# Performance work log

Measured on AMD Instinct MI355X. Metric: run time of the kernel, lower is better.

Reference implementation:

```python
import jax, jax.numpy as jnp
import numpy as np

NL, D, DI, N, R, K = 32, 256, 512, 16, 16, 4   # layers, d_model, d_inner, d_state, dt_rank, d_conv
V, FF, BATCH, L = 4096, 1024, 32, 256


def _mamba_layer(x, p):
    # x: (B, L, D). One pre-norm Mamba block with residual: x + mamba(LN(x)).
    ln_w, ln_b, in_w, cw, cb, xp_w, dtw, dtb, A_log, Dskip, out_w = p
    mu = x.mean(-1, keepdims=True)
    var = ((x - mu) ** 2).mean(-1, keepdims=True)
    h = (x - mu) / jnp.sqrt(var + 1e-5) * ln_w + ln_b
    xz = jnp.einsum('bld,ed->ble', h, in_w)            # (B, L, 2*DI)
    xm, z = jnp.split(xz, 2, axis=-1)
    seq = xm.shape[1]
    # causal depthwise conv1d, kernel K, then SiLU
    xpad = jnp.pad(xm, ((0, 0), (K - 1, 0), (0, 0)))
    xc = sum(xpad[:, k:k + seq] * cw[:, k] for k in range(K)) + cb
    xc = jax.nn.silu(xc)
    dbc = jnp.einsum('ble,fe->blf', xc, xp_w)          # (B, L, R+2N)
    dt, Bm, Cm = jnp.split(dbc, [R, R + N], axis=-1)
    dt = jax.nn.softplus(jnp.einsum('blr,er->ble', dt, dtw) + dtb)  # (B, L, DI)
    A = -jnp.exp(A_log)                                # (DI, N)

    def step(hs, inp):
        dt_t, B_t, C_t, x_t = inp                      # (B,DI),(B,N),(B,N),(B,DI)
        dA = jnp.exp(dt_t[..., None] * A)              # (B, DI, N)
        hs = hs * dA + (dt_t * x_t)[..., None] * B_t[:, None, :]
        return hs, jnp.einsum('ben,bn->be', hs, C_t)

    h0 = jnp.zeros((xc.shape[0], DI, N), xc.dtype)
    _, ys = jax.lax.scan(step, h0, (dt.swapaxes(0, 1), Bm.swapaxes(0, 1), Cm.swapaxes(0, 1), xc.swapaxes(0, 1)))
    y = ys.swapaxes(0, 1) + xc * Dskip
    y = y * jax.nn.silu(z)
    return x + jnp.einsum('ble,de->bld', y, out_w)


def _stack_forward(x, params):
    return jax.lax.scan(lambda c, p: (jax.checkpoint(_mamba_layer)(c, p), None), x, params)[0]


def setup_inputs() -> dict:
    key = jax.random.key(0)
    ks = jax.random.split(key, 12)
    rn = lambda k, shape, s=0.02: jax.random.normal(k, shape, jnp.float32) * s
    return {
        'token_ids': jax.random.randint(ks[0], (BATCH, L), 0, V),
        'emb': rn(ks[1], (V, D)),
        'ln_w': jnp.ones((NL, D)), 'ln_b': jnp.zeros((NL, D)),
        'in_proj_w': rn(ks[2], (NL, 2 * DI, D)),
        'conv_w': rn(ks[3], (NL, DI, K), 0.1), 'conv_b': jnp.zeros((NL, DI)),
        'x_proj_w': rn(ks[4], (NL, R + 2 * N, DI)),
        'dt_w': rn(ks[5], (NL, DI, R), 0.1),
        'dt_b': jnp.full((NL, DI), float(np.log(np.expm1(0.01))), jnp.float32),
        'A_log': jnp.broadcast_to(jnp.log(jnp.arange(1, N + 1, dtype=jnp.float32)), (NL, DI, N)) + 0.0,
        'Dskip': jnp.ones((NL, DI)),
        'out_proj_w': rn(ks[6], (NL, D, DI)),
        'W1': rn(ks[7], (FF, D)), 'b1': jnp.zeros((FF,)),
        'W2': rn(ks[8], (V, FF)), 'b2': jnp.zeros((V,)),
    }


def reference(token_ids, emb, ln_w, ln_b, in_proj_w, conv_w, conv_b, x_proj_w, dt_w, dt_b, A_log, Dskip, out_proj_w, W1, b1, W2, b2):
    x = emb[token_ids]                                  # (B, L, D)
    params = (ln_w, ln_b, in_proj_w, conv_w, conv_b, x_proj_w, dt_w, dt_b, A_log, Dskip, out_proj_w)
    x = _stack_forward(x, params)                       # 32 stacked Mamba blocks
    h = jax.nn.relu(x @ W1.T + b1)
    return h @ W2.T + b2                                # (B, L, V) logits
```

## Files before the change

kernel.cpp:

```cpp
#include <hip/hip_runtime.h>
#include <hip/hip_bf16.h>
#include <cstdint>
#include <cstddef>


typedef __bf16 v8bf __attribute__((ext_vector_type(8)));
typedef float  v4f  __attribute__((ext_vector_type(4)));

__device__ __forceinline__ void async_copy16(const void* g, void* l) {
  __builtin_amdgcn_global_load_lds((const __attribute__((address_space(1))) void*)g,
                                   (__attribute__((address_space(3))) void*)l, 16, 0, 0);
}

__device__ __forceinline__ float bf(__bf16 v) { return (float)v; }

constexpr size_t OFF_WIN  = 0;
constexpr size_t OFF_WXP  = 16777216;
constexpr size_t OFF_WOUT = 18350080;
constexpr size_t OFF_WW1  = 26738688;
constexpr size_t OFF_WW2  = 27262976;
constexpr size_t OFF_X    = 35651584;
constexpr size_t OFF_H    = 44040192;
constexpr size_t OFF_XZ   = 48234496;
constexpr size_t OFF_DBC  = 65011712;
constexpr size_t OFF_PART = 66584576;
constexpr size_t OFF_SS   = 82313216;
constexpr size_t OFF_A2   = 83296256;

__global__ __launch_bounds__(256)
void f2b_multi(const float* __restrict__ s0, const float* __restrict__ s1,
               const float* __restrict__ s2, const float* __restrict__ s3,
               const float* __restrict__ s4, const float* __restrict__ s5,
               char* __restrict__ ws) {
  size_t i = (size_t)blockIdx.x * 256 + threadIdx.x;
  if (i < 8388608) { ((__bf16*)(ws + OFF_WIN))[i] = (__bf16)s0[i]; return; }
  i -= 8388608;
  if (i < 786432)  { ((__bf16*)(ws + OFF_WXP))[i] = (__bf16)s1[i]; return; }
  i -= 786432;
  if (i < 4194304) { ((__bf16*)(ws + OFF_WOUT))[i] = (__bf16)s2[i]; return; }
  i -= 4194304;
  if (i < 262144)  { ((__bf16*)(ws + OFF_WW1))[i] = (__bf16)s3[i]; return; }
  i -= 262144;
  if (i < 4194304) { ((__bf16*)(ws + OFF_WW2))[i] = (__bf16)s4[i]; return; }
  i -= 4194304;
  ((float*)(ws + OFF_A2))[i] = -1.4426950408889634f * __expf(s5[i]);
}

__global__ __launch_bounds__(256) void f2b_k(const float* __restrict__ X,
                                             __bf16* __restrict__ O) {
  size_t i = (size_t)blockIdx.x * 256 + threadIdx.x;
  O[i] = (__bf16)X[i];
}

__global__ __launch_bounds__(256)
void embed_ln_k(const int* __restrict__ tok, const float* __restrict__ emb,
                const float* __restrict__ w, const float* __restrict__ b,
                float* __restrict__ X, __bf16* __restrict__ H) {
  int row = blockIdx.x;
  int t   = threadIdx.x;
  float v = emb[(size_t)tok[row] * 256 + t];
  X[(size_t)row * 256 + t] = v;
  float s = v, q = v * v;
  #pragma unroll
  for (int o = 32; o > 0; o >>= 1) { s += __shfl_xor(s, o); q += __shfl_xor(q, o); }
  __shared__ float ss[4], qq[4];
  int wv = t >> 6;
  if ((t & 63) == 0) { ss[wv] = s; qq[wv] = q; }
  __syncthreads();
  s = ss[0] + ss[1] + ss[2] + ss[3];
  q = qq[0] + qq[1] + qq[2] + qq[3];
  float mu  = s * (1.f / 256.f);
  float var = q * (1.f / 256.f) - mu * mu;
  float r   = rsqrtf(var + 1e-5f);
  H[(size_t)row * 256 + t] = (__bf16)((v - mu) * r * w[t] + b[t]);
}

template <int EPI>
__global__ __launch_bounds__(256, 2)
void gemm_bt(const __bf16* __restrict__ A, const __bf16* __restrict__ W,
             void* outp, const float* __restrict__ bias, int M, int N, int K) {
  __shared__ __align__(16) __bf16 sA[128 * 32];
  __shared__ __align__(16) __bf16 sB[128 * 32];
  const int tid  = threadIdx.x;
  const int bm0  = blockIdx.y << 7;
  const int bn0  = blockIdx.x << 7;
  const int lane = tid & 63;
  const int wv   = tid >> 6;
  const int wm   = (wv >> 1) << 6;
  const int wn   = (wv & 1) << 6;
  const int lr   = lane & 15;
  const int lk   = lane >> 4;

  v4f acc[4][4] = {};

  const int r0 = tid >> 2;
  const int c0 = (tid & 3) << 3;
  const int wbase = (tid & ~63) << 3;

  const __bf16* gA0 = A + (size_t)(bm0 + r0) * K + c0;
  const __bf16* gA1 = A + (size_t)(bm0 + 64 + r0) * K + c0;
  const __bf16* gB0 = W + (size_t)(bn0 + r0) * K + c0;
  const __bf16* gB1 = W + (size_t)(bn0 + 64 + r0) * K + c0;

  for (int kk = 0; kk < K; kk += 32) {
    async_copy16(gA0 + kk, sA + wbase);
    async_copy16(gA1 + kk, sA + 2048 + wbase);
    async_copy16(gB0 + kk, sB + wbase);
    async_copy16(gB1 + kk, sB + 2048 + wbase);
    __syncthreads();
    v8bf af[4], bfr[4];
    #pragma unroll
    for (int i = 0; i < 4; ++i)
      af[i] = *(const v8bf*)(sA + ((wm + i * 16 + lr) << 5) + (lk << 3));
    #pragma unroll
    for (int j = 0; j < 4; ++j)
      bfr[j] = *(const v8bf*)(sB + ((wn + j * 16 + lr) << 5) + (lk << 3));
    #pragma unroll
    for (int i = 0; i < 4; ++i)
      #pragma unroll
      for (int j = 0; j < 4; ++j)
        acc[i][j] = __builtin_amdgcn_mfma_f32_16x16x32_bf16(af[i], bfr[j], acc[i][j], 0, 0, 0);
    __syncthreads();
  }

  #pragma unroll
  for (int i = 0; i < 4; ++i) {
    #pragma unroll
    for (int j = 0; j < 4; ++j) {
      int gc = bn0 + wn + j * 16 + lr;
      #pragma unroll
      for (int v = 0; v < 4; ++v) {
        int gr = bm0 + wm + i * 16 + (lk << 2) + v;
        float val = acc[i][j][v];
        size_t idx = (size_t)gr * N + gc;
        if (EPI == 0) {
          ((__bf16*)outp)[idx] = (__bf16)val;
        } else if (EPI == 1) {
          val += bias[gc]; val = fmaxf(val, 0.f);
          ((__bf16*)outp)[idx] = (__bf16)val;
        } else {
          ((float*)outp)[idx] = val + bias[gc];
        }
      }
    }
  }
}

__global__ __launch_bounds__(512, 4)
void convscan1_k(const __bf16* __restrict__ XZ,
                 const float* __restrict__ cw, const float* __restrict__ cb,
                 const __bf16* __restrict__ Wxp,
                 const float* __restrict__ dtw, const float* __restrict__ dtb,
                 const float* __restrict__ A2,
                 float* __restrict__ DBC,
                 float* __restrict__ PART, float* __restrict__ SS) {
  __shared__ __align__(16) __bf16 sXC[16 * 512];
  __shared__ __align__(16) float  sDBC[16 * 48];
  const int tid = threadIdx.x;
  const int c   = blockIdx.x >> 5;
  const int b   = blockIdx.x & 31;
  const int bl0 = b * 256 + c * 16;

  {
    const int r  = tid >> 5;
    const int ec = tid & 31;
    #pragma unroll
    for (int j = 0; j < 2; ++j) {
      const int e = (ec << 3) + (j << 8);
      v4f cw4[8];
      #pragma unroll
      for (int jj = 0; jj < 8; ++jj) cw4[jj] = *(const v4f*)(cw + (size_t)(e + jj) * 4);
      float a[8];
      #pragma unroll
      for (int jj = 0; jj < 8; ++jj) a[jj] = cb[e + jj];
      #pragma unroll
      for (int k = 0; k < 4; ++k) {
        if (c > 0 || r + k >= 3) {
          const v8bf xv = *(const v8bf*)(XZ + (size_t)(bl0 + r + k - 3) * 1024 + e);
          #pragma unroll
          for (int jj = 0; jj < 8; ++jj) a[jj] += bf(xv[jj]) * cw4[jj][k];
        }
      }
      v8bf outv;
      #pragma unroll
      for (int jj = 0; jj < 8; ++jj) {
        float s = a[jj] / (1.f + __expf(-a[jj]));
        outv[jj] = (__bf16)s;
      }
      const int cbk = (e >> 3) ^ (r & 7);
      *(v8bf*)(sXC + r * 512 + (cbk << 3)) = outv;
    }
  }
  __syncthreads();

  if (tid < 192) {
    const int w = tid >> 6, lane = tid & 63, lr = lane & 15, lk = lane >> 4;
    v4f acc = {};
    for (int kk = 0; kk < 512; kk += 32) {
      const v8bf bfr = *(const v8bf*)(Wxp + (size_t)(w * 16 + lr) * 512 + kk + (lk << 3));
      const int cbk = (((kk >> 3) + lk) ^ (lr & 7));
      const v8bf af = *(const v8bf*)(sXC + lr * 512 + (cbk << 3));
      acc = __builtin_amdgcn_mfma_f32_16x16x32_bf16(af, bfr, acc, 0, 0, 0);
    }
    const int gc = w * 16 + lr;
    #pragma unroll
    for (int v = 0; v < 4; ++v)
      sDBC[((lk << 2) + v) * 48 + gc] = acc[v];
  }
  __syncthreads();

  if (tid < 192)
    *(v4f*)(DBC + (size_t)bl0 * 48 + tid * 4) = *(const v4f*)(sDBC + tid * 4);

  if (c < 15) {
    const int e = tid;
    v4f a2[4], wd[4];
    #pragma unroll
    for (int q = 0; q < 4; ++q) {
      a2[q] = *(const v4f*)(A2  + (size_t)e * 16 + q * 4);
      wd[q] = *(const v4f*)(dtw + (size_t)e * 16 + q * 4);
    }
    const float bias = dtb[e];
    float part[16];
    #pragma unroll
    for (int n = 0; n < 16; ++n) part[n] = 0.f;
    float S = 0.f;
    for (int tt = 0; tt < 16; ++tt) {
      const v4f* dp = (const v4f*)(sDBC + tt * 48);
      float dtv = bias;
      {
        const v4f d0 = dp[0], d1 = dp[1], d2 = dp[2], d3 = dp[3];
        #pragma unroll
        for (int r = 0; r < 4; ++r)
          dtv += d0[r] * wd[0][r] + d1[r] * wd[1][r] + d2[r] * wd[2][r] + d3[r] * wd[3][r];
      }
      dtv = (dtv > 20.f) ? dtv : log1pf(__expf(dtv));
      const float x = bf(sXC[tt * 512 + (((e >> 3) ^ (tt & 7)) << 3) + (e & 7)]);
      const float dtx = dtv * x;
      S += dtv;
      {
        const v4f bv0 = dp[4], bv1 = dp[5], bv2 = dp[6], bv3 = dp[7];
        #pragma unroll
        for (int v = 0; v < 4; ++v) {
          part[v]      = part[v]      * exp2f(dtv * a2[0][v]) + dtx * bv0[v];
          part[4 + v]  = part[4 + v]  * exp2f(dtv * a2[1][v]) + dtx * bv1[v];
          part[8 + v]  = part[8 + v]  * exp2f(dtv * a2[2][v]) + dtx * bv2[v];
          part[12 + v] = part[12 + v] * exp2f(dtv * a2[3][v]) + dtx * bv3[v];
        }
      }
    }
    const size_t o = (((size_t)c * 32 + b) * 512 + e) * 16;
    #pragma unroll
    for (int rq = 0; rq < 4; ++rq) {
      v4f p;
      #pragma unroll
      for (int v = 0; v < 4; ++v) p[v] = part[rq * 4 + v];
      *(v4f*)(PART + o + rq * 4) = p;
    }
    SS[((size_t)c * 32 + b) * 512 + e] = S;
  }
}

__global__ __launch_bounds__(512, 4)
void scan2out_k(const __bf16* __restrict__ XZ,
                const float* __restrict__ cw, const float* __restrict__ cb,
                const float* __restrict__ DBC,
                const float* __restrict__ dtw, const float* __restrict__ dtb,
                const float* __restrict__ A2, const float* __restrict__ Dskip,
                const float* __restrict__ PART, const float* __restrict__ SS,
                const __bf16* __restrict__ Wout,
                const float* __restrict__ lnw, const float* __restrict__ lnb,
                float* __restrict__ X, __bf16* __restrict__ H) {
  __shared__ __align__(16) __bf16 sY[16 * 520];
  __shared__ __align__(16) __bf16 sB[256 * 32];
  __shared__ float sSum[8][16], sSq[8][16];
  const int tid = threadIdx.x;
  const int c   = blockIdx.x >> 5;
  const int b   = blockIdx.x & 31;
  const int bl0 = b * 256 + c * 16;
  const int e   = tid;

  v4f a2[4], wd[4];
  #pragma unroll
  for (int q = 0; q < 4; ++q) {
    a2[q] = *(const v4f*)(A2  + (size_t)e * 16 + q * 4);
    wd[q] = *(const v4f*)(dtw + (size_t)e * 16 + q * 4);
  }
  const float bias = dtb[e];
  const float Dsk  = Dskip[e];
  const v4f   cwv  = *(const v4f*)(cw + (size_t)e * 4);
  const float cbe  = cb[e];

  float h[16];
  #pragma unroll
  for (int n = 0; n < 16; ++n) h[n] = 0.f;
  for (int cc = 0; cc < c; ++cc) {
    const float S  = SS[((size_t)cc * 32 + b) * 512 + e];
    const size_t o = (((size_t)cc * 32 + b) * 512 + e) * 16;
    #pragma unroll
    for (int rq = 0; rq < 4; ++rq) {
      const v4f p = *(const v4f*)(PART + o + rq * 4);
      #pragma unroll
      for (int v = 0; v < 4; ++v)
        h[rq * 4 + v] = h[rq * 4 + v] * exp2f(a2[rq][v] * S) + p[v];
    }
  }

  float w0 = 0.f, w1 = 0.f, w2 = 0.f;
  if (c > 0) {
    w0 = bf(XZ[(size_t)(bl0 - 3) * 1024 + e]);
    w1 = bf(XZ[(size_t)(bl0 - 2) * 1024 + e]);
    w2 = bf(XZ[(size_t)(bl0 - 1) * 1024 + e]);
  }

  for (int tt = 0; tt < 16; ++tt) {
    const float xt = bf(XZ[(size_t)(bl0 + tt) * 1024 + e]);
    float a = cbe + w0 * cwv[0] + w1 * cwv[1] + w2 * cwv[2] + xt * cwv[3];
    const float x = a / (1.f + __expf(-a));
    w0 = w1; w1 = w2; w2 = xt;
    const v4f* dp = (const v4f*)(DBC + (size_t)(bl0 + tt) * 48);
    float dtv = bias;
    {
      const v4f d0 = dp[0], d1 = dp[1], d2 = dp[2], d3 = dp[3];
      #pragma unroll
      for (int r = 0; r < 4; ++r)
        dtv += d0[r] * wd[0][r] + d1[r] * wd[1][r] + d2[r] * wd[2][r] + d3[r] * wd[3][r];
    }
    dtv = (dtv > 20.f) ? dtv : log1pf(__expf(dtv));
    const float dtx = dtv * x;
    float y = 0.f;
    {
      const v4f bv0 = dp[4], bv1 = dp[5], bv2 = dp[6], bv3 = dp[7];
      const v4f cv0 = dp[8], cv1 = dp[9], cv2 = dp[10], cv3 = dp[11];
      #pragma unroll
      for (int v = 0; v < 4; ++v) {
        h[v]      = h[v]      * exp2f(dtv * a2[0][v]) + dtx * bv0[v];  y += h[v]      * cv0[v];
        h[4 + v]  = h[4 + v]  * exp2f(dtv * a2[1][v]) + dtx * bv1[v];  y += h[4 + v]  * cv1[v];
        h[8 + v]  = h[8 + v]  * exp2f(dtv * a2[2][v]) + dtx * bv2[v];  y += h[8 + v]  * cv2[v];
        h[12 + v] = h[12 + v] * exp2f(dtv * a2[3][v]) + dtx * bv3[v];  y += h[12 + v] * cv3[v];
      }
    }
    const float z  = bf(XZ[(size_t)(bl0 + tt) * 1024 + 512 + e]);
    const float sg = z / (1.f + __expf(-z));
    sY[tt * 520 + e] = (__bf16)((y + x * Dsk) * sg);
  }
  __syncthreads();

  const int w = tid >> 6, lane = tid & 63, lr = lane & 15, lk = lane >> 4;
  const int wn = w << 5;
  v4f acc[2] = {};
  for (int kk = 0; kk < 512; kk += 32) {
    async_copy16(Wout + (size_t)(tid >> 2) * 512 + ((tid & 3) << 3) + kk,
                 sB + ((tid & ~63) << 3));
    async_copy16(Wout + (size_t)(128 + (tid >> 2)) * 512 + ((tid & 3) << 3) + kk,
                 sB + 4096 + ((tid & ~63) << 3));
    __syncthreads();
    const v8bf af = *(const v8bf*)(sY + lr * 520 + kk + (lk << 3));
    #pragma unroll
    for (int j = 0; j < 2; ++j) {
      const v8bf bfr = *(const v8bf*)(sB + ((wn + j * 16 + lr) << 5) + (lk << 3));
      acc[j] = __builtin_amdgcn_mfma_f32_16x16x32_bf16(af, bfr, acc[j], 0, 0, 0);
    }
    __syncthreads();
  }

  float s2[4], q2[4];
  #pragma unroll
  for (int v = 0; v < 4; ++v) {
    const int gr = bl0 + (lk << 2) + v;
    float s = 0.f, q = 0.f;
    #pragma unroll
    for (int j = 0; j < 2; ++j) {
      const int gc = wn + j * 16 + lr;
      float val = X[(size_t)gr * 256 + gc] + acc[j][v];
      acc[j][v] = val;
      s += val; q += val * val;
    }
    #pragma unroll
    for (int o = 8; o > 0; o >>= 1) { s += __shfl_xor(s, o); q += __shfl_xor(q, o); }
    s2[v] = s; q2[v] = q;
  }
  if (lr == 0) {
    #pragma unroll
    for (int v = 0; v < 4; ++v) {
      const int row = (lk << 2) + v;
      sSum[w][row] = s2[v];
      sSq[w][row]  = q2[v];
    }
  }
  __syncthreads();
  #pragma unroll
  for (int v = 0; v < 4; ++v) {
    const int row = (lk << 2) + v;
    float S = 0.f, Q = 0.f;
    #pragma unroll
    for (int ww = 0; ww < 8; ++ww) { S += sSum[ww][row]; Q += sSq[ww][row]; }
    const float mu   = S * (1.f / 256.f);
    const float var  = Q * (1.f / 256.f) - mu * mu;
    const float rinv = rsqrtf(var + 1e-5f);
    const int gr = bl0 + row;
    #pragma unroll
    for (int j = 0; j < 2; ++j) {
      const int gc = wn + j * 16 + lr;
      const float val = acc[j][v];
      X[(size_t)gr * 256 + gc] = val;
      H[(size_t)gr * 256 + gc] = (__bf16)((val - mu) * rinv * lnw[gc] + lnb[gc]);
    }
  }
}

extern "C" void kernel_launch(void* const* d_in, const int* in_sizes, int n_in,
                              void* d_out, int out_size, void* d_ws, size_t ws_size,
                              hipStream_t stream) {
  const int*   tok  = (const int*)d_in[0];
  const float* emb  = (const float*)d_in[1];
  const float* lnw  = (const float*)d_in[2];
  const float* lnb  = (const float*)d_in[3];
  const float* inw  = (const float*)d_in[4];
  const float* cw   = (const float*)d_in[5];
  const float* cb   = (const float*)d_in[6];
  const float* xpw  = (const float*)d_in[7];
  const float* dtw  = (const float*)d_in[8];
  const float* dtb  = (const float*)d_in[9];
  const float* alog = (const float*)d_in[10];
  const float* dsk  = (const float*)d_in[11];
  const float* outw = (const float*)d_in[12];
  const float* W1   = (const float*)d_in[13];
  const float* b1   = (const float*)d_in[14];
  const float* W2   = (const float*)d_in[15];
  const float* b2   = (const float*)d_in[16];

  char* ws = (char*)d_ws;
  __bf16* WIN   = (__bf16*)(ws + OFF_WIN);
  __bf16* WXP   = (__bf16*)(ws + OFF_WXP);
  __bf16* WOUT  = (__bf16*)(ws + OFF_WOUT);
  __bf16* WW1   = (__bf16*)(ws + OFF_WW1);
  __bf16* WW2   = (__bf16*)(ws + OFF_WW2);
  float*  X     = (float*)(ws + OFF_X);
  __bf16* H     = (__bf16*)(ws + OFF_H);
  __bf16* XZ    = (__bf16*)(ws + OFF_XZ);
  float*  DBC   = (float*)(ws + OFF_DBC);
  float*  PART  = (float*)(ws + OFF_PART);
  float*  SS    = (float*)(ws + OFF_SS);
  float*  A2    = (float*)(ws + OFF_A2);
  __bf16* XB    = (__bf16*)(ws + OFF_PART);
  __bf16* HH    = (__bf16*)(ws + OFF_PART + 8388608);

  f2b_multi<<<70656, 256, 0, stream>>>(inw, xpw, outw, W1, W2, alog, ws);
  embed_ln_k<<<8192, 256, 0, stream>>>(tok, emb, lnw, lnb, X, H);

  for (int l = 0; l < 32; ++l) {
    const float*  cw_l   = cw   + (size_t)l * 512 * 4;
    const float*  cb_l   = cb   + (size_t)l * 512;
    const __bf16* xpw_l  = WXP  + (size_t)l * 48 * 512;
    const float*  dtw_l  = dtw  + (size_t)l * 512 * 16;
    const float*  dtb_l  = dtb  + (size_t)l * 512;
    const float*  A2_l   = A2   + (size_t)l * 512 * 16;
    const float*  dsk_l  = dsk  + (size_t)l * 512;
    const __bf16* inw_l  = WIN  + (size_t)l * 1024 * 256;
    const __bf16* outw_l = WOUT + (size_t)l * 256 * 512;
    const int lnx = (l + 1 < 32) ? l + 1 : 31;

    gemm_bt<0><<<dim3(8, 64), 256, 0, stream>>>(H, inw_l, XZ, nullptr, 8192, 1024, 256);
    convscan1_k<<<512, 512, 0, stream>>>(XZ, cw_l, cb_l, xpw_l, dtw_l, dtb_l,
                                         A2_l, DBC, PART, SS);
    scan2out_k<<<512, 512, 0, stream>>>(XZ, cw_l, cb_l, DBC, dtw_l, dtb_l,
                                        A2_l, dsk_l, PART, SS, outw_l,
                                        lnw + (size_t)lnx * 256,
                                        lnb + (size_t)lnx * 256, X, H);
  }

  f2b_k<<<8192, 256, 0, stream>>>(X, XB);
  gemm_bt<1><<<dim3(8, 64), 256, 0, stream>>>(XB, WW1, HH, b1, 8192, 1024, 256);
  gemm_bt<2><<<dim3(32, 64), 256, 0, stream>>>(HH, WW2, (float*)d_out, b2, 8192, 4096, 1024);
}
```

Baseline: 4.244 ms.

## Fuse per-layer Mamba kernels into a persistent megakernel with grid barriers

Replaces the 96 per-layer launches (in_proj GEMM, conv+chunk scan, scan+out_proj) with one persistent kernel of 512 blocks that loops over all 32 layers and separates the phases with a hierarchical atomic grid barrier. The conv/xproj results (xc in fp32, dbc) now stay in shared memory between the chunk-scan phase and the final scan phase, so the DBC global buffer and the conv recomputation go away. The cost is that every block must be co-resident for the barrier to work, and the barrier has a timeout escape that could silently break correctness if that fails. The in_proj GEMM now uses 512-thread blocks computing 128x128 tiles, a different tiling from the old GEMM.

```diff
diff --git a/kernel.cpp b/kernel.cpp
--- a/kernel.cpp
+++ b/kernel.cpp
@@ -22,16 +22,22 @@
 constexpr size_t OFF_X    = 35651584;
 constexpr size_t OFF_H    = 44040192;
 constexpr size_t OFF_XZ   = 48234496;
-constexpr size_t OFF_DBC  = 65011712;
 constexpr size_t OFF_PART = 66584576;
 constexpr size_t OFF_SS   = 82313216;
 constexpr size_t OFF_A2   = 83296256;
+constexpr size_t OFF_BAR  = 84344832;
 
 __global__ __launch_bounds__(256)
 void f2b_multi(const float* __restrict__ s0, const float* __restrict__ s1,
                const float* __restrict__ s2, const float* __restrict__ s3,
                const float* __restrict__ s4, const float* __restrict__ s5,
                char* __restrict__ ws) {
+  if (blockIdx.x == 0) {
+    int* bar = (int*)(ws + OFF_BAR);
+    bar[threadIdx.x] = 0;
+    bar[threadIdx.x + 256] = 0;
+    if (threadIdx.x < 32) bar[threadIdx.x + 512] = 0;
+  }
   size_t i = (size_t)blockIdx.x * 256 + threadIdx.x;
   if (i < 8388608) { ((__bf16*)(ws + OFF_WIN))[i] = (__bf16)s0[i]; return; }
   i -= 8388608;
@@ -146,266 +152,328 @@
   }
 }
 
-__global__ __launch_bounds__(512, 4)
-void convscan1_k(const __bf16* __restrict__ XZ,
-                 const float* __restrict__ cw, const float* __restrict__ cb,
-                 const __bf16* __restrict__ Wxp,
-                 const float* __restrict__ dtw, const float* __restrict__ dtb,
-                 const float* __restrict__ A2,
-                 float* __restrict__ DBC,
-                 float* __restrict__ PART, float* __restrict__ SS) {
-  __shared__ __align__(16) __bf16 sXC[16 * 512];
-  __shared__ __align__(16) float  sDBC[16 * 48];
-  const int tid = threadIdx.x;
-  const int c   = blockIdx.x >> 5;
-  const int b   = blockIdx.x & 31;
-  const int bl0 = b * 256 + c * 16;
-
-  {
-    const int r  = tid >> 5;
-    const int ec = tid & 31;
-    #pragma unroll
-    for (int j = 0; j < 2; ++j) {
-      const int e = (ec << 3) + (j << 8);
-      v4f cw4[8];
-      #pragma unroll
-      for (int jj = 0; jj < 8; ++jj) cw4[jj] = *(const v4f*)(cw + (size_t)(e + jj) * 4);
-      float a[8];
-      #pragma unroll
-      for (int jj = 0; jj < 8; ++jj) a[jj] = cb[e + jj];
-      #pragma unroll
-      for (int k = 0; k < 4; ++k) {
-        if (c > 0 || r + k >= 3) {
-          const v8bf xv = *(const v8bf*)(XZ + (size_t)(bl0 + r + k - 3) * 1024 + e);
-          #pragma unroll
-          for (int jj = 0; jj < 8; ++jj) a[jj] += bf(xv[jj]) * cw4[jj][k];
-        }
-      }
-      v8bf outv;
-      #pragma unroll
-      for (int jj = 0; jj < 8; ++jj) {
-        float s = a[jj] / (1.f + __expf(-a[jj]));
-        outv[jj] = (__bf16)s;
-      }
-      const int cbk = (e >> 3) ^ (r & 7);
-      *(v8bf*)(sXC + r * 512 + (cbk << 3)) = outv;
+__device__ __forceinline__ void gbar(int* BAR, int ph) {
+  __syncthreads();
+  if (threadIdx.x == 0) {
+    __threadfence();
+    int* cg   = BAR + ((blockIdx.x >> 4) << 4);
+    int* root = BAR + 512;
+    int* phs  = BAR + 528;
+    bool last = false;
+    int p = __hip_atomic_fetch_add(cg, 1, __ATOMIC_ACQ_REL, __HIP_MEMORY_SCOPE_AGENT);
+    if (p == 15) {
+      int q = __hip_atomic_fetch_add(root, 1, __ATOMIC_ACQ_REL, __HIP_MEMORY_SCOPE_AGENT);
+      last = (q == 31);
     }
+    if (last) {
+      #pragma unroll 1
+      for (int i = 0; i <= 32; ++i)
+        __hip_atomic_store(BAR + i * 16, 0, __ATOMIC_RELAXED, __HIP_MEMORY_SCOPE_AGENT);
+      __hip_atomic_store(phs, ph, __ATOMIC_RELEASE, __HIP_MEMORY_SCOPE_AGENT);
+    } else {
+      long long t0 = clock64();
+      while (__hip_atomic_load(phs, __ATOMIC_ACQUIRE, __HIP_MEMORY_SCOPE_AGENT) < ph) {
+        if (clock64() - t0 > 5000000LL) break;
+      }
+    }
+    __threadfence();
   }
   __syncthreads();
-
-  if (tid < 192) {
-    const int w = tid >> 6, lane = tid & 63, lr = lane & 15, lk = lane >> 4;
-    v4f acc = {};
-    for (int kk = 0; kk < 512; kk += 32) {
-      const v8bf bfr = *(const v8bf*)(Wxp + (size_t)(w * 16 + lr) * 512 + kk + (lk << 3));
-      const int cbk = (((kk >> 3) + lk) ^ (lr & 7));
-      const v8bf af = *(const v8bf*)(sXC + lr * 512 + (cbk << 3));
-      acc = __builtin_amdgcn_mfma_f32_16x16x32_bf16(af, bfr, acc, 0, 0, 0);
+}
+
+struct MegaP {
+  const __bf16 *WIN, *WXP, *WOUT;
+  const float *cw, *cb, *dtw, *dtb, *A2v, *dsk, *lnw, *lnb;
+  float *X; __bf16 *H; __bf16 *XZ; float *PART; float *SS; int *BAR;
+};
+
+__global__ __launch_bounds__(512, 4) void mamba_mega(MegaP P) {
+  __shared__ __align__(16) char sMem[69888];
+  __bf16* const sXC  = (__bf16*)sMem;
+  __bf16* const sY   = (__bf16*)sMem;
+  float*  const sXCf = (float*)(sMem + 16640);
+  float*  const sDBC = (float*)(sMem + 49408);
+  __bf16* const sB3  = (__bf16*)(sMem + 52480);
+  float*  const sSum = (float*)(sMem + 68864);
+  float*  const sSq  = (float*)(sMem + 69376);
+  __bf16* const sA1  = (__bf16*)sMem;
+  __bf16* const sB1  = (__bf16*)(sMem + 8192);
+
+  const int tid = threadIdx.x;
+  const int bid = blockIdx.x;
+  const int c   = bid >> 5, b = bid & 31;
+  const int bl0 = b * 256 + c * 16;
+  const int bm0 = (bid >> 3) << 7;
+  const int bn0 = (bid & 7) << 7;
+  const int lane = tid & 63, wv = tid >> 6;
+  const int lr = lane & 15, lk = lane >> 4;
+  int ph = 0;
+
+  for (int l = 0; l < 32; ++l) {
+    const __bf16* Wi  = P.WIN  + (size_t)l * 262144;
+    const __bf16* Wx  = P.WXP  + (size_t)l * 24576;
+    const __bf16* Wo  = P.WOUT + (size_t)l * 131072;
+    const float* cwL  = P.cw  + (size_t)l * 2048;
+    const float* cbL  = P.cb  + (size_t)l * 512;
+    const float* dtwL = P.dtw + (size_t)l * 8192;
+    const float* dtbL = P.dtb + (size_t)l * 512;
+    const float* A2L  = P.A2v + (size_t)l * 8192;
+    const float* dskL = P.dsk + (size_t)l * 512;
+    const int lnx = (l + 1 < 32) ? l + 1 : 31;
+    const float* lnwL = P.lnw + (size_t)lnx * 256;
+    const float* lnbL = P.lnb + (size_t)lnx * 256;
+
+    {
+      const int wm  = (wv >> 2) << 6;
+      const int wnc = (((wv >> 1) & 1) << 6) + ((wv & 1) << 5);
+      v4f acc[4][2] = {};
+      const int r0 = tid >> 2, c0 = (tid & 3) << 3;
+      const int wbase = (tid & ~63) << 3;
+      const __bf16* gA = P.H + (size_t)(bm0 + r0) * 256 + c0;
+      const __bf16* gB = Wi  + (size_t)(bn0 + r0) * 256 + c0;
+      for (int kk = 0; kk < 256; kk += 32) {
+        async_copy16(gA + kk, sA1 + wbase);
+        async_copy16(gB + kk, sB1 + wbase);
+        __syncthreads();
+        v8bf af[4], bfr[2];
+        #pragma unroll
+        for (int i = 0; i < 4; ++i)
+          af[i] = *(const v8bf*)(sA1 + ((wm + i * 16 + lr) << 5) + (lk << 3));
+        #pragma unroll
+        for (int j = 0; j < 2; ++j)
+          bfr[j] = *(const v8bf*)(sB1 + ((wnc + j * 16 + lr) << 5) + (lk << 3));
+        #pragma unroll
+        for (int i = 0; i < 4; ++i)
+          #pragma unroll
+          for (int j = 0; j < 2; ++j)
+            acc[i][j] = __builtin_amdgcn_mfma_f32_16x16x32_bf16(af[i], bfr[j], acc[i][j], 0, 0, 0);
+        __syncthreads();
+      }
+      #pragma unroll
+      for (int i = 0; i < 4; ++i)
+        #pragma unroll
+        for (int j = 0; j < 2; ++j)
+          #pragma unroll
+          for (int v = 0; v < 4; ++v)
+            P.XZ[(size_t)(bm0 + wm + i * 16 + (lk << 2) + v) * 1024 +
+                 (bn0 + wnc + j * 16 + lr)] = (__bf16)acc[i][j][v];
     }
-    const int gc = w * 16 + lr;
-    #pragma unroll
-    for (int v = 0; v < 4; ++v)
-      sDBC[((lk << 2) + v) * 48 + gc] = acc[v];
-  }
-  __syncthreads();
-
-  if (tid < 192)
-    *(v4f*)(DBC + (size_t)bl0 * 48 + tid * 4) = *(const v4f*)(sDBC + tid * 4);
-
-  if (c < 15) {
-    const int e = tid;
-    v4f a2[4], wd[4];
-    #pragma unroll
-    for (int q = 0; q < 4; ++q) {
-      a2[q] = *(const v4f*)(A2  + (size_t)e * 16 + q * 4);
-      wd[q] = *(const v4f*)(dtw + (size_t)e * 16 + q * 4);
+    gbar(P.BAR, ++ph);
+
+    {
+      const int r = tid >> 5, ec = tid & 31;
+      #pragma unroll
+      for (int j = 0; j < 2; ++j) {
+        const int e = (ec << 3) + (j << 8);
+        v4f cw4[8];
+        #pragma unroll
+        for (int jj = 0; jj < 8; ++jj) cw4[jj] = *(const v4f*)(cwL + (size_t)(e + jj) * 4);
+        float a[8];
+        #pragma unroll
+        for (int jj = 0; jj < 8; ++jj) a[jj] = cbL[e + jj];
+        #pragma unroll
+        for (int k = 0; k < 4; ++k) {
+          if (c > 0 || r + k >= 3) {
+            const v8bf xv = *(const v8bf*)(P.XZ + (size_t)(bl0 + r + k - 3) * 1024 + e);
+            #pragma unroll
+            for (int jj = 0; jj < 8; ++jj) a[jj] += bf(xv[jj]) * cw4[jj][k];
+          }
+        }
+        v8bf outv; v4f f0, f1;
+        #pragma unroll
+        for (int jj = 0; jj < 8; ++jj) {
+          const float s = a[jj] / (1.f + __expf(-a[jj]));
+          outv[jj] = (__bf16)s;
+          if (jj < 4) f0[jj] = s; else f1[jj - 4] = s;
+        }
+        const int cbk = (e >> 3) ^ (r & 7);
+        *(v8bf*)(sXC + r * 512 + (cbk << 3)) = outv;
+        *(v4f*)(sXCf + r * 512 + e)     = f0;
+        *(v4f*)(sXCf + r * 512 + e + 4) = f1;
+      }
+      __syncthreads();
+      if (tid < 192) {
+        const int w = tid >> 6;
+        v4f acc = {};
+        for (int kk = 0; kk < 512; kk += 32) {
+          const v8bf bfr = *(const v8bf*)(Wx + (size_t)(w * 16 + lr) * 512 + kk + (lk << 3));
+          const int cbk = (((kk >> 3) + lk) ^ (lr & 7));
+          const v8bf af = *(const v8bf*)(sXC + lr * 512 + (cbk << 3));
+          acc = __builtin_amdgcn_mfma_f32_16x16x32_bf16(af, bfr, acc, 0, 0, 0);
+        }
+        const int gc = w * 16 + lr;
+        #pragma unroll
+        for (int v = 0; v < 4; ++v)
+          sDBC[((lk << 2) + v) * 48 + gc] = acc[v];
+      }
+      __syncthreads();
+      if (c < 15) {
+        const int e = tid;
+        v4f a2v[4], wd[4];
+        #pragma unroll
+        for (int q = 0; q < 4; ++q) {
+          a2v[q] = *(const v4f*)(A2L  + (size_t)e * 16 + q * 4);
+          wd[q]  = *(const v4f*)(dtwL + (size_t)e * 16 + q * 4);
+        }
+        const float bias = dtbL[e];
+        float part[16];
+        #pragma unroll
+        for (int n = 0; n < 16; ++n) part[n] = 0.f;
+        float S = 0.f;
+        for (int tt = 0; tt < 16; ++tt) {
+          const v4f* dp = (const v4f*)(sDBC + tt * 48);
+          float dtv = bias;
+          {
+            const v4f d0 = dp[0], d1 = dp[1], d2 = dp[2], d3 = dp[3];
+            #pragma unroll
+            for (int r2 = 0; r2 < 4; ++r2)
+              dtv += d0[r2] * wd[0][r2] + d1[r2] * wd[1][r2] + d2[r2] * wd[2][r2] + d3[r2] * wd[3][r2];
+          }
+          dtv = (dtv > 20.f) ? dtv : log1pf(__expf(dtv));
+          const float x = sXCf[tt * 512 + e];
+          const float dtx = dtv * x;
+          S += dtv;
+          {
+            const v4f bv0 = dp[4], bv1 = dp[5], bv2 = dp[6], bv3 = dp[7];
+            #pragma unroll
+            for (int v = 0; v < 4; ++v) {
+              part[v]      = part[v]      * exp2f(dtv * a2v[0][v]) + dtx * bv0[v];
+              part[4 + v]  = part[4 + v]  * exp2f(dtv * a2v[1][v]) + dtx * bv1[v];
+              part[8 + v]  = part[8 + v]  * exp2f(dtv * a2v[2][v]) + dtx * bv2[v];
+              part[12 + v] = part[12 + v] * exp2f(dtv * a2v[3][v]) + dtx * bv3[v];
+            }
+          }
+        }
+        const size_t o = (((size_t)c * 32 + b) * 512 + e) * 16;
+        #pragma unroll
+        for (int rq = 0; rq < 4; ++rq) {
+          v4f p;
+          #pragma unroll
+          for (int v = 0; v < 4; ++v) p[v] = part[rq * 4 + v];
+          *(v4f*)(P.PART + o + rq * 4) = p;
+        }
+        P.SS[((size_t)c * 32 + b) * 512 + e] = S;
+      }
     }
-    const float bias = dtb[e];
-    float part[16];
-    #pragma unroll
-    for (int n = 0; n < 16; ++n) part[n] = 0.f;
-    float S = 0.f;
-    for (int tt = 0; tt < 16; ++tt) {
-      const v4f* dp = (const v4f*)(sDBC + tt * 48);
-      float dtv = bias;
-      {
-        const v4f d0 = dp[0], d1 = dp[1], d2 = dp[2], d3 = dp[3];
-        #pragma unroll
-        for (int r = 0; r < 4; ++r)
-          dtv += d0[r] * wd[0][r] + d1[r] * wd[1][r] + d2[r] * wd[2][r] + d3[r] * wd[3][r];
-      }
-      dtv = (dtv > 20.f) ? dtv : log1pf(__expf(dtv));
-      const float x = bf(sXC[tt * 512 + (((e >> 3) ^ (tt & 7)) << 3) + (e & 7)]);
-      const float dtx = dtv * x;
-      S += dtv;
-      {
-        const v4f bv0 = dp[4], bv1 = dp[5], bv2 = dp[6], bv3 = dp[7];
+    gbar(P.BAR, ++ph);
+
+    {
+      const int e = tid;
+      v4f a2v[4], wd[4];
+      #pragma unroll
+      for (int q = 0; q < 4; ++q) {
+        a2v[q] = *(const v4f*)(A2L  + (size_t)e * 16 + q * 4);
+        wd[q]  = *(const v4f*)(dtwL + (size_t)e * 16 + q * 4);
+      }
+      const float bias = dtbL[e];
+      const float Dsk  = dskL[e];
+      float h[16];
+      #pragma unroll
+      for (int n = 0; n < 16; ++n) h[n] = 0.f;
+      for (int cc = 0; cc < c; ++cc) {
+        const float S  = P.SS[((size_t)cc * 32 + b) * 512 + e];
+        const size_t o = (((size_t)cc * 32 + b) * 512 + e) * 16;
+        #pragma unroll
+        for (int rq = 0; rq < 4; ++rq) {
+          const v4f p = *(const v4f*)(P.PART + o + rq * 4);
+          #pragma unroll
+          for (int v = 0; v < 4; ++v)
+            h[rq * 4 + v] = h[rq * 4 + v] * exp2f(a2v[rq][v] * S) + p[v];
+        }
+      }
+      for (int tt = 0; tt < 16; ++tt) {
+        const float x = sXCf[tt * 512 + e];
+        const v4f* dp = (const v4f*)(sDBC + tt * 48);
+        float dtv = bias;
+        {
+          const v4f d0 = dp[0], d1 = dp[1], d2 = dp[2], d3 = dp[3];
+          #pragma unroll
+          for (int r2 = 0; r2 < 4; ++r2)
+            dtv += d0[r2] * wd[0][r2] + d1[r2] * wd[1][r2] + d2[r2] * wd[2][r2] + d3[r2] * wd[3][r2];
+        }
+        dtv = (dtv > 20.f) ? dtv : log1pf(__expf(dtv));
+        const float dtx = dtv * x;
+        float y = 0.f;
+        {
+          const v4f bv0 = dp[4], bv1 = dp[5], bv2 = dp[6], bv3 = dp[7];
+          const v4f cv0 = dp[8], cv1 = dp[9], cv2 = dp[10], cv3 = dp[11];
+          #pragma unroll
+          for (int v = 0; v < 4; ++v) {
+            h[v]      = h[v]      * exp2f(dtv * a2v[0][v]) + dtx * bv0[v];  y += h[v]      * cv0[v];
+            h[4 + v]  = h[4 + v]  * exp2f(dtv * a2v[1][v]) + dtx * bv1[v];  y += h[4 + v]  * cv1[v];
+            h[8 + v]  = h[8 + v]  * exp2f(dtv * a2v[2][v]) + dtx * bv2[v];  y += h[8 + v]  * cv2[v];
+            h[12 + v] = h[12 + v] * exp2f(dtv * a2v[3][v]) + dtx * bv3[v];  y += h[12 + v] * cv3[v];
+          }
+        }
+        const float z  = bf(P.XZ[(size_t)(bl0 + tt) * 1024 + 512 + e]);
+        const float sg = z / (1.f + __expf(-z));
+        sY[tt * 520 + e] = (__bf16)((y + x * Dsk) * sg);
+      }
+      __syncthreads();
+
+      const int wn = wv << 5;
+      v4f acc[2] = {};
+      for (int kk = 0; kk < 512; kk += 32) {
+        async_copy16(Wo + (size_t)(tid >> 2) * 512 + ((tid & 3) << 3) + kk,
+                     sB3 + ((tid & ~63) << 3));
+        async_copy16(Wo + (size_t)(128 + (tid >> 2)) * 512 + ((tid & 3) << 3) + kk,
+                     sB3 + 4096 + ((tid & ~63) << 3));
+        __syncthreads();
+        const v8bf af = *(const v8bf*)(sY + lr * 520 + kk + (lk << 3));
+        #pragma unroll
+        for (int j = 0; j < 2; ++j) {
+          const v8bf bfr = *(const v8bf*)(sB3 + ((wn + j * 16 + lr) << 5) + (lk << 3));
+          acc[j] = __builtin_amdgcn_mfma_f32_16x16x32_bf16(af, bfr, acc[j], 0, 0, 0);
+        }
+        __syncthreads();
+      }
+
+      float s2[4], q2[4];
+      #pragma unroll
+      for (int v = 0; v < 4; ++v) {
+        const int gr = bl0 + (lk << 2) + v;
+        float s = 0.f, q = 0.f;
+        #pragma unroll
+        for (int j = 0; j < 2; ++j) {
+          const int gc = wn + j * 16 + lr;
+          float val = P.X[(size_t)gr * 256 + gc] + acc[j][v];
+          acc[j][v] = val;
+          s += val; q += val * val;
+        }
+        #pragma unroll
+        for (int o = 8; o > 0; o >>= 1) { s += __shfl_xor(s, o); q += __shfl_xor(q, o); }
+        s2[v] = s; q2[v] = q;
+      }
+      if (lr == 0) {
         #pragma unroll
         for (int v = 0; v < 4; ++v) {
-          part[v]      = part[v]      * exp2f(dtv * a2[0][v]) + dtx * bv0[v];
-          part[4 + v]  = part[4 + v]  * exp2f(dtv * a2[1][v]) + dtx * bv1[v];
-          part[8 + v]  = part[8 + v]  * exp2f(dtv * a2[2][v]) + dtx * bv2[v];
-          part[12 + v] = part[12 + v] * exp2f(dtv * a2[3][v]) + dtx * bv3[v];
-        }
-      }
+          const int row = (lk << 2) + v;
+          sSum[wv * 16 + row] = s2[v];
+          sSq[wv * 16 + row]  = q2[v];
+        }
+      }
+      __syncthreads();
+      #pragma unroll
+      for (int v = 0; v < 4; ++v) {
+        const int row = (lk << 2) + v;
+        float S = 0.f, Q = 0.f;
+        #pragma unroll
+        for (int ww = 0; ww < 8; ++ww) { S += sSum[ww * 16 + row]; Q += sSq[ww * 16 + row]; }
+        const float mu   = S * (1.f / 256.f);
+        const float var  = Q * (1.f / 256.f) - mu * mu;
+        const float rinv = rsqrtf(var + 1e-5f);
+        const int gr = bl0 + row;
+        #pragma unroll
+        for (int j = 0; j < 2; ++j) {
+          const int gc = wn + j * 16 + lr;
+          const float val = acc[j][v];
+          P.X[(size_t)gr * 256 + gc] = val;
+          P.H[(size_t)gr * 256 + gc] = (__bf16)((val - mu) * rinv * lnwL[gc] + lnbL[gc]);
+        }
+      }
+      __syncthreads();
     }
-    const size_t o = (((size_t)c * 32 + b) * 512 + e) * 16;
-    #pragma unroll
-    for (int rq = 0; rq < 4; ++rq) {
-      v4f p;
-      #pragma unroll
-      for (int v = 0; v < 4; ++v) p[v] = part[rq * 4 + v];
-      *(v4f*)(PART + o + rq * 4) = p;
-    }
-    SS[((size_t)c * 32 + b) * 512 + e] = S;
-  }
-}
-
-__global__ __launch_bounds__(512, 4)
-void scan2out_k(const __bf16* __restrict__ XZ,
-                const float* __restrict__ cw, const float* __restrict__ cb,
-                const float* __restrict__ DBC,
-                const float* __restrict__ dtw, const float* __restrict__ dtb,
-                const float* __restrict__ A2, const float* __restrict__ Dskip,
-                const float* __restrict__ PART, const float* __restrict__ SS,
-                const __bf16* __restrict__ Wout,
-                const float* __restrict__ lnw, const float* __restrict__ lnb,
-                float* __restrict__ X, __bf16* __restrict__ H) {
-  __shared__ __align__(16) __bf16 sY[16 * 520];
-  __shared__ __align__(16) __bf16 sB[256 * 32];
-  __shared__ float sSum[8][16], sSq[8][16];
-  const int tid = threadIdx.x;
-  const int c   = blockIdx.x >> 5;
-  const int b   = blockIdx.x & 31;
-  const int bl0 = b * 256 + c * 16;
-  const int e   = tid;
-
-  v4f a2[4], wd[4];
-  #pragma unroll
-  for (int q = 0; q < 4; ++q) {
-    a2[q] = *(const v4f*)(A2  + (size_t)e * 16 + q * 4);
-    wd[q] = *(const v4f*)(dtw + (size_t)e * 16 + q * 4);
-  }
-  const float bias = dtb[e];
-  const float Dsk  = Dskip[e];
-  const v4f   cwv  = *(const v4f*)(cw + (size_t)e * 4);
-  const float cbe  = cb[e];
-
-  float h[16];
-  #pragma unroll
-  for (int n = 0; n < 16; ++n) h[n] = 0.f;
-  for (int cc = 0; cc < c; ++cc) {
-    const float S  = SS[((size_t)cc * 32 + b) * 512 + e];
-    const size_t o = (((size_t)cc * 32 + b) * 512 + e) * 16;
-    #pragma unroll
-    for (int rq = 0; rq < 4; ++rq) {
-      const v4f p = *(const v4f*)(PART + o + rq * 4);
-      #pragma unroll
-      for (int v = 0; v < 4; ++v)
-        h[rq * 4 + v] = h[rq * 4 + v] * exp2f(a2[rq][v] * S) + p[v];
-    }
-  }
-
-  float w0 = 0.f, w1 = 0.f, w2 = 0.f;
-  if (c > 0) {
-    w0 = bf(XZ[(size_t)(bl0 - 3) * 1024 + e]);
-    w1 = bf(XZ[(size_t)(bl0 - 2) * 1024 + e]);
-    w2 = bf(XZ[(size_t)(bl0 - 1) * 1024 + e]);
-  }
-
-  for (int tt = 0; tt < 16; ++tt) {
-    const float xt = bf(XZ[(size_t)(bl0 + tt) * 1024 + e]);
-    float a = cbe + w0 * cwv[0] + w1 * cwv[1] + w2 * cwv[2] + xt * cwv[3];
-    const float x = a / (1.f + __expf(-a));
-    w0 = w1; w1 = w2; w2 = xt;
-    const v4f* dp = (const v4f*)(DBC + (size_t)(bl0 + tt) * 48);
-    float dtv = bias;
-    {
-      const v4f d0 = dp[0], d1 = dp[1], d2 = dp[2], d3 = dp[3];
-      #pragma unroll
-      for (int r = 0; r < 4; ++r)
-        dtv += d0[r] * wd[0][r] + d1[r] * wd[1][r] + d2[r] * wd[2][r] + d3[r] * wd[3][r];
-    }
-    dtv = (dtv > 20.f) ? dtv : log1pf(__expf(dtv));
-    const float dtx = dtv * x;
-    float y = 0.f;
-    {
-      const v4f bv0 = dp[4], bv1 = dp[5], bv2 = dp[6], bv3 = dp[7];
-      const v4f cv0 = dp[8], cv1 = dp[9], cv2 = dp[10], cv3 = dp[11];
-      #pragma unroll
-      for (int v = 0; v < 4; ++v) {
-        h[v]      = h[v]      * exp2f(dtv * a2[0][v]) + dtx * bv0[v];  y += h[v]      * cv0[v];
-        h[4 + v]  = h[4 + v]  * exp2f(dtv * a2[1][v]) + dtx * bv1[v];  y += h[4 + v]  * cv1[v];
-        h[8 + v]  = h[8 + v]  * exp2f(dtv * a2[2][v]) + dtx * bv2[v];  y += h[8 + v]  * cv2[v];
-        h[12 + v] = h[12 + v] * exp2f(dtv * a2[3][v]) + dtx * bv3[v];  y += h[12 + v] * cv3[v];
-      }
-    }
-    const float z  = bf(XZ[(size_t)(bl0 + tt) * 1024 + 512 + e]);
-    const float sg = z / (1.f + __expf(-z));
-    sY[tt * 520 + e] = (__bf16)((y + x * Dsk) * sg);
-  }
-  __syncthreads();
-
-  const int w = tid >> 6, lane = tid & 63, lr = lane & 15, lk = lane >> 4;
-  const int wn = w << 5;
-  v4f acc[2] = {};
-  for (int kk = 0; kk < 512; kk += 32) {
-    async_copy16(Wout + (size_t)(tid >> 2) * 512 + ((tid & 3) << 3) + kk,
-                 sB + ((tid & ~63) << 3));
-    async_copy16(Wout + (size_t)(128 + (tid >> 2)) * 512 + ((tid & 3) << 3) + kk,
-                 sB + 4096 + ((tid & ~63) << 3));
-    __syncthreads();
-    const v8bf af = *(const v8bf*)(sY + lr * 520 + kk + (lk << 3));
-    #pragma unroll
-    for (int j = 0; j < 2; ++j) {
-      const v8bf bfr = *(const v8bf*)(sB + ((wn + j * 16 + lr) << 5) + (lk << 3));
-      acc[j] = __builtin_amdgcn_mfma_f32_16x16x32_bf16(af, bfr, acc[j], 0, 0, 0);
-    }
-    __syncthreads();
-  }
-
-  float s2[4], q2[4];
-  #pragma unroll
-  for (int v = 0; v < 4; ++v) {
-    const int gr = bl0 + (lk << 2) + v;
-    float s = 0.f, q = 0.f;
-    #pragma unroll
-    for (int j = 0; j < 2; ++j) {
-      const int gc = wn + j * 16 + lr;
-      float val = X[(size_t)gr * 256 + gc] + acc[j][v];
-      acc[j][v] = val;
-      s += val; q += val * val;
-    }
-    #pragma unroll
-    for (int o = 8; o > 0; o >>= 1) { s += __shfl_xor(s, o); q += __shfl_xor(q, o); }
-    s2[v] = s; q2[v] = q;
-  }
-  if (lr == 0) {
-    #pragma unroll
-    for (int v = 0; v < 4; ++v) {
-      const int row = (lk << 2) + v;
-      sSum[w][row] = s2[v];
-      sSq[w][row]  = q2[v];
-    }
-  }
-  __syncthreads();
-  #pragma unroll
-  for (int v = 0; v < 4; ++v) {
-    const int row = (lk << 2) + v;
-    float S = 0.f, Q = 0.f;
-    #pragma unroll
-    for (int ww = 0; ww < 8; ++ww) { S += sSum[ww][row]; Q += sSq[ww][row]; }
-    const float mu   = S * (1.f / 256.f);
-    const float var  = Q * (1.f / 256.f) - mu * mu;
-    const float rinv = rsqrtf(var + 1e-5f);
-    const int gr = bl0 + row;
-    #pragma unroll
-    for (int j = 0; j < 2; ++j) {
-      const int gc = wn + j * 16 + lr;
-      const float val = acc[j][v];
-      X[(size_t)gr * 256 + gc] = val;
-      H[(size_t)gr * 256 + gc] = (__bf16)((val - mu) * rinv * lnw[gc] + lnb[gc]);
-    }
+    gbar(P.BAR, ++ph);
   }
 }
 
@@ -439,36 +507,22 @@
   float*  X     = (float*)(ws + OFF_X);
   __bf16* H     = (__bf16*)(ws + OFF_H);
   __bf16* XZ    = (__bf16*)(ws + OFF_XZ);
-  float*  DBC   = (float*)(ws + OFF_DBC);
   float*  PART  = (float*)(ws + OFF_PART);
   float*  SS    = (float*)(ws + OFF_SS);
   float*  A2    = (float*)(ws + OFF_A2);
+  int*    BAR   = (int*)(ws + OFF_BAR);
   __bf16* XB    = (__bf16*)(ws + OFF_PART);
   __bf16* HH    = (__bf16*)(ws + OFF_PART + 8388608);
 
   f2b_multi<<<70656, 256, 0, stream>>>(inw, xpw, outw, W1, W2, alog, ws);
   embed_ln_k<<<8192, 256, 0, stream>>>(tok, emb, lnw, lnb, X, H);
 
-  for (int l = 0; l < 32; ++l) {
-    const float*  cw_l   = cw   + (size_t)l * 512 * 4;
-    const float*  cb_l   = cb   + (size_t)l * 512;
-    const __bf16* xpw_l  = WXP  + (size_t)l * 48 * 512;
-    const float*  dtw_l  = dtw  + (size_t)l * 512 * 16;
-    const float*  dtb_l  = dtb  + (size_t)l * 512;
-    const float*  A2_l   = A2   + (size_t)l * 512 * 16;
-    const float*  dsk_l  = dsk  + (size_t)l * 512;
-    const __bf16* inw_l  = WIN  + (size_t)l * 1024 * 256;
-    const __bf16* outw_l = WOUT + (size_t)l * 256 * 512;
-    const int lnx = (l + 1 < 32) ? l + 1 : 31;
-
-    gemm_bt<0><<<dim3(8, 64), 256, 0, stream>>>(H, inw_l, XZ, nullptr, 8192, 1024, 256);
-    convscan1_k<<<512, 512, 0, stream>>>(XZ, cw_l, cb_l, xpw_l, dtw_l, dtb_l,
-                                         A2_l, DBC, PART, SS);
-    scan2out_k<<<512, 512, 0, stream>>>(XZ, cw_l, cb_l, DBC, dtw_l, dtb_l,
-                                        A2_l, dsk_l, PART, SS, outw_l,
-                                        lnw + (size_t)lnx * 256,
-                                        lnb + (size_t)lnx * 256, X, H);
-  }
+  MegaP mp;
+  mp.WIN = WIN; mp.WXP = WXP; mp.WOUT = WOUT;
+  mp.cw = cw; mp.cb = cb; mp.dtw = dtw; mp.dtb = dtb;
+  mp.A2v = A2; mp.dsk = dsk; mp.lnw = lnw; mp.lnb = lnb;
+  mp.X = X; mp.H = H; mp.XZ = XZ; mp.PART = PART; mp.SS = SS; mp.BAR = BAR;
+  mamba_mega<<<512, 512, 0, stream>>>(mp);
 
   f2b_k<<<8192, 256, 0, stream>>>(X, XB);
   gemm_bt<1><<<dim3(8, 64), 256, 0, stream>>>(XB, WW1, HH, b1, 8192, 1024, 256);
```

After: 14.19 ms. +234.4%, slower.
